# Optimization experiments

Measured on AMD Instinct MI355X. Metric: run time of the kernel, lower is better.

Reference implementation:

```python
import jax, jax.numpy as jnp
import numpy as np
import math

B, T, DIM = 4, 4096, 1024
HID = int(DIM * 1.5)  # 1536
K = 4                  # conv kernel size
S = 16                 # num_slots
D = 384                # slot_dim


def setup_inputs() -> dict:
    key = jax.random.key(0)
    ks = jax.random.split(key, 16)
    inp = {
        "x": jax.random.normal(ks[0], (B, T, DIM), jnp.float32),
        "input_w": jax.random.normal(ks[1], (2 * HID, DIM), jnp.float32) * DIM ** -0.5,
        "conv_w": jax.random.normal(ks[2], (HID, K), jnp.float32) * K ** -0.5,
        "conv_b": jnp.zeros((HID,), jnp.float32),
        "gates_w": jax.random.normal(ks[3], (2 * HID, HID), jnp.float32) * HID ** -0.5,
        "gates_b": jnp.zeros((2 * HID,), jnp.float32),
        "forget_base": jnp.linspace(-4.323, -9.0, HID).astype(jnp.float32),
        "output_w": jax.random.normal(ks[4], (DIM, HID), jnp.float32) * HID ** -0.5,
        "memory_slots": jax.random.normal(ks[5], (S, D), jnp.float32) * 0.02,
        "wq_w": jax.random.normal(ks[6], (D, D), jnp.float32) * 0.02,
        "wk_w": jax.random.normal(ks[7], (D, HID), jnp.float32) * 0.02,
        "wv_w": jax.random.normal(ks[8], (D, HID), jnp.float32) * 0.02,
        "wg_w": jax.random.normal(ks[9], (1, HID), jnp.float32) * 0.02,
        "rq_w": jax.random.normal(ks[10], (D, HID), jnp.float32) * 0.02,
        "rk_w": jax.random.normal(ks[11], (D, D), jnp.float32) * 0.02,
        "rv_w": jax.random.normal(ks[12], (HID, D), jnp.float32) * 0.02,
    }
    return inp


def _causal_dwconv(x, w, b):
    # x: [B,T,H], w: [H,K], b: [H]; torch Conv1d(padding=K-1) then [:, :T] == causal
    xp = jnp.pad(x, ((0, 0), (K - 1, 0), (0, 0)))
    taps = jnp.stack([xp[:, j:j + T, :] for j in range(K)], axis=-1)  # [B,T,H,K]
    return jnp.einsum('bthk,hk->bth', taps, w) + b


def _scan(alpha, x):
    # h_t = alpha_t * h_{t-1} + x_t, elementwise over channels; along axis 1 (time)
    def combine(c1, c2):
        a1, b1 = c1
        a2, b2 = c2
        return a1 * a2, a2 * b1 + b2
    return jax.lax.associative_scan(combine, (alpha, x), axis=1)[1]


def reference(x, input_w, conv_w, conv_b, gates_w, gates_b, forget_base, output_w,
              memory_slots, wq_w, wk_w, wv_w, wg_w, rq_w, rk_w, rv_w):
    L = T // S  # segment length
    proj = x @ input_w.T                       # [B,T,2H]
    gate, xh = proj[..., :HID], proj[..., HID:]
    xh = _causal_dwconv(xh, conv_w, conv_b)    # [B,T,H]
    g = xh @ gates_w.T + gates_b               # [B,T,2H]
    forget, inp = g[..., :HID], g[..., HID:]
    alpha = jnp.exp(-8.0 * jax.nn.softplus(forget_base) * jax.nn.sigmoid(forget))
    xh = jnp.sqrt(1.0 - alpha ** 2 + 1e-6) * jax.nn.sigmoid(inp) * xh
    h = _scan(alpha, xh)                       # [B,T,H]
    xh = gate * jax.nn.sigmoid(gate) * xh      # silu-gated

    # ---- write_memory(xh) ----
    xseg = xh.reshape(B, S, L, HID)
    q = memory_slots @ wq_w.T                  # [S,D]
    kmat = jnp.einsum('bslh,dh->bsld', xseg, wk_w)
    vmat = jnp.einsum('bslh,dh->bsld', xseg, wv_w)
    qk = jnp.einsum('sd,bsld->bsl', q, kmat) / math.sqrt(D)
    attn = jax.nn.softmax(qk, axis=-1)
    mem = jnp.einsum('bsl,bsld->bsd', attn, vmat)  # [B,S,D]

    # ---- read_memory(gelu(xh)*h, mem) ----
    xr = jax.nn.gelu(xh, approximate=False) * h    # [B,T,H]
    rq = xr @ rq_w.T                               # [B,T,D]
    rk = mem @ rk_w.T                              # [B,S,D]
    rv = mem @ rv_w.T                              # [B,S,H]
    qk2 = jnp.einsum('btd,bsd->bts', rq, rk) / math.sqrt(D)
    seg = jnp.arange(T) // L
    mask = seg[:, None] <= jnp.arange(S)[None, :]  # [T,S]
    qk2 = jnp.where(mask[None], qk2, -jnp.inf)
    attn2 = jax.nn.softmax(qk2, axis=-1)
    out = jnp.einsum('bts,bsh->bth', attn2, rv)
    out = jax.nn.sigmoid(xr @ wg_w.T) * out        # write_gate on xr
    return out @ output_w.T                        # [B,T,DIM]
```

## Files before the change

kernel.cpp:

```cpp
#include <hip/hip_runtime.h>
#include <math.h>

#define BB 4
#define TT 4096
#define DIMW 1024
#define HID 1536
#define HID2 3072
#define KC 4
#define SSEG 16
#define LSEG 256
#define DD 384
#define NCH 64
#define CHL 64
#define TH  ((size_t)TT*(size_t)HID)

typedef _Float16 h8 __attribute__((ext_vector_type(8)));
typedef float f4 __attribute__((ext_vector_type(4)));

__device__ __forceinline__ void hsplit(float a, _Float16& h0, _Float16& h1)
{
    _Float16 t = (_Float16)a;
    float tf = (float)t;
    if (fabsf(tf) < 6.103515625e-05f) { t = (_Float16)0.f; tf = 0.f; }
    h0 = t;
    h1 = (_Float16)((a - tf) * 2048.0f);
}

__device__ __forceinline__ void gl_lds16(const _Float16* g, _Float16* l)
{
    __builtin_amdgcn_global_load_lds(
        (const __attribute__((address_space(1))) unsigned int*)g,
        (__attribute__((address_space(3))) unsigned int*)l,
        16, 0, 0);
}

__global__ __launch_bounds__(256) void split2t(const float* __restrict__ src,
                                               _Float16* __restrict__ dst,
                                               int R, int Kd, size_t ps)
{
    __shared__ float tile[64][65];
    const int tid = threadIdx.x;
    const int bx = blockIdx.x;
    const int by = blockIdx.y;
    {
        const int lr = tid >> 2;
        const int lc = (tid & 3) * 16;
        const float* s = src + (size_t)(by * 64 + lr) * Kd + bx * 64 + lc;
#pragma unroll
        for (int e = 0; e < 16; e++) tile[lr][lc + e] = s[e];
    }
    __syncthreads();
    const int c = tid >> 5;
    const int r0 = tid & 31;
#pragma unroll
    for (int rr = 0; rr < 2; rr++) {
        const int r = r0 + rr * 32;
        h8 h0v, h1v;
#pragma unroll
        for (int e = 0; e < 8; e++) {
            _Float16 a0, a1;
            hsplit(tile[r][c * 8 + e], a0, a1);
            h0v[e] = a0; h1v[e] = a1;
        }
        const size_t didx = ((size_t)(bx * 8 + c) * R + by * 64 + r) * 8;
        *(h8*)(dst + didx) = h0v;
        *(h8*)(dst + ps + didx) = h1v;
    }
}

__global__ __launch_bounds__(256) void catkv_kernel(const float* __restrict__ wk,
                                                    const float* __restrict__ wv,
                                                    float* __restrict__ wkv)
{
    const int half = DD * HID;
    int i = blockIdx.x * 256 + threadIdx.x;
    if (i < half) wkv[i] = wk[i];
    else if (i < 2 * half) wkv[i] = wv[i - half];
}

template<int MODE, int TM, int TN>
__global__ __launch_bounds__(256, 2) void gemm_mfma(
    const _Float16* __restrict__ Ap, size_t aps,
    const _Float16* __restrict__ Wp, size_t wps,
    float* __restrict__ C0, float* __restrict__ C1,
    const float* __restrict__ X,
    int M, int Nout, int Kd)
{
    constexpr int MI = TM / 32;
    constexpr int NI = TN / 32;
    constexpr int API = TM / 16;
    constexpr int BPI = TN / 16;
    constexpr int ATOT = 2 * API;
    constexpr int NISS = ATOT + 2 * BPI;

    __shared__ _Float16 Als[2][2][TM * 32];
    __shared__ _Float16 Bls[2][2][TN * 32];

    const int tid = threadIdx.x;
    const int lane = tid & 63;
    const int wv = tid >> 6;
    const int wr = wv >> 1, wc = wv & 1;
    const int lr = lane & 15, lg = lane >> 4;

    int bx = blockIdx.x, by = blockIdx.y;
    {
        const int gx = gridDim.x;
        const int nwg = gx * gridDim.y;
        if ((nwg & 7) == 0) {
            int wg = by * gx + bx;
            wg = (wg & 7) * (nwg >> 3) + (wg >> 3);
            bx = wg % gx; by = wg / gx;
        }
    }
    const int m0 = bx * TM, n0 = by * TN;

    f4 acc1[MI][NI], acc2[MI][NI];
#pragma unroll
    for (int i = 0; i < MI; i++)
#pragma unroll
        for (int j = 0; j < NI; j++) {
            acc1[i][j] = (f4){0.f, 0.f, 0.f, 0.f};
            acc2[i][j] = (f4){0.f, 0.f, 0.f, 0.f};
        }

    auto stage = [&](int kq0, int buf) {
#pragma unroll
        for (int j = 0; j < NISS / 4; j++) {
            const int i = j * 4 + wv;
            if (i < ATOT) {
                const int pl = i / API, s = i - pl * API;
                const int kc = (s * 64) / TM, r0 = (s * 64) % TM;
                const _Float16* g = Ap + pl * aps
                    + ((size_t)(kq0 + kc) * M + m0 + r0) * 8 + lane * 8;
                gl_lds16(g, &Als[buf][pl][(kc * TM + r0) * 8]);
            } else {
                const int jj = i - ATOT;
                const int pl = jj / BPI, s = jj - pl * BPI;
                const int kc = (s * 64) / TN, r0 = (s * 64) % TN;
                const _Float16* g = Wp + pl * wps
                    + ((size_t)(kq0 + kc) * Nout + n0 + r0) * 8 + lane * 8;
                gl_lds16(g, &Bls[buf][pl][(kc * TN + r0) * 8]);
            }
        }
    };

    stage(0, 0);
    __syncthreads();

    const int NS = Kd / 32;
    for (int t = 0; t < NS; t++) {
        const int buf = t & 1;
        if (t + 1 < NS) stage((t + 1) * 4, buf ^ 1);

        h8 af0[MI], af1[MI];
#pragma unroll
        for (int mi = 0; mi < MI; mi++) {
            const int arow = wr * (TM / 2) + mi * 16 + lr;
            af0[mi] = *(const h8*)&Als[buf][0][(lg * TM + arow) * 8];
            af1[mi] = *(const h8*)&Als[buf][1][(lg * TM + arow) * 8];
        }
#pragma unroll
        for (int ni = 0; ni < NI; ni++) {
            const int brow = wc * (TN / 2) + ni * 16 + lr;
            h8 b0 = *(const h8*)&Bls[buf][0][(lg * TN + brow) * 8];
            h8 b1 = *(const h8*)&Bls[buf][1][(lg * TN + brow) * 8];
#pragma unroll
            for (int mi = 0; mi < MI; mi++) {
                acc1[mi][ni] = __builtin_amdgcn_mfma_f32_16x16x32_f16(af0[mi], b0, acc1[mi][ni], 0, 0, 0);
                acc2[mi][ni] = __builtin_amdgcn_mfma_f32_16x16x32_f16(af1[mi], b0, acc2[mi][ni], 0, 0, 0);
                acc2[mi][ni] = __builtin_amdgcn_mfma_f32_16x16x32_f16(af0[mi], b1, acc2[mi][ni], 0, 0, 0);
            }
        }
        __syncthreads();
    }

#pragma unroll
    for (int mi = 0; mi < MI; mi++) {
#pragma unroll
        for (int ni = 0; ni < NI; ni++) {
#pragma unroll
            for (int r = 0; r < 4; r++) {
                const float v = acc1[mi][ni][r] + acc2[mi][ni][r] * 4.8828125e-4f;
                const int m = m0 + wr * (TM / 2) + mi * 16 + lg * 4 + r;
                const int n = n0 + wc * (TN / 2) + ni * 16 + lr;
                if constexpr (MODE == 1) {
                    if (n < HID) C0[(size_t)m * HID + n] = v;
                    else         C1[(size_t)m * HID + (n - HID)] = v;
                } else if constexpr (MODE == 2) {
                    double g = (double)v;
                    double val = (g / (1.0 + exp(-g))) * (double)X[(size_t)m * Nout + n];
                    C0[(size_t)m * Nout + n] = (float)val;
                } else {
                    C0[(size_t)m * Nout + n] = v;
                }
            }
        }
    }
}

template<int MODE, int TM, int TN>
__global__ __launch_bounds__(256) void gemm32(const float* __restrict__ A,
                                              const float* __restrict__ W,
                                              float* __restrict__ C0,
                                              float* __restrict__ C1,
                                              const float* __restrict__ X,
                                              int M, int Nout, int Kd)
{
    constexpr int GM = TM / 64;
    constexpr int GN = TN / 64;
    constexpr int AF4 = TM * 4;
    constexpr int WF4 = TN * 4;
    constexpr int ALOOP = (AF4 + 255) / 256;
    constexpr int WLOOP = (WF4 + 255) / 256;

    __shared__ float As[16][TM];
    __shared__ float Bs[16][TN];

    const int tid = threadIdx.x;
    const int m0 = blockIdx.x * TM;
    const int n0 = blockIdx.y * TN;
    const int tx = tid & 15, ty = tid >> 4;

    float acc[GM * 4][GN * 4];
#pragma unroll
    for (int i = 0; i < GM * 4; i++)
#pragma unroll
        for (int j = 0; j < GN * 4; j++) acc[i][j] = 0.0f;

    float4 aReg[ALOOP], wReg[WLOOP];

    auto issueLoads = [&](int k0) {
#pragma unroll
        for (int u = 0; u < ALOOP; u++) {
            const int idx = tid + u * 256;
            float4 v = make_float4(0.f, 0.f, 0.f, 0.f);
            if (idx < AF4) {
                const int row = idx >> 2, kq = (idx & 3) * 4;
                const long ar = (long)(m0 + row);
                if (ar < M) v = *(const float4*)(A + ar * (long)Kd + (k0 + kq));
            }
            aReg[u] = v;
        }
#pragma unroll
        for (int u = 0; u < WLOOP; u++) {
            const int idx = tid + u * 256;
            float4 v = make_float4(0.f, 0.f, 0.f, 0.f);
            if (idx < WF4) {
                const int row = idx >> 2, kq = (idx & 3) * 4;
                const long wr = (long)(n0 + row);
                v = *(const float4*)(W + wr * (long)Kd + (k0 + kq));
            }
            wReg[u] = v;
        }
    };
    auto writeLDS = [&]() {
#pragma unroll
        for (int u = 0; u < ALOOP; u++) {
            const int idx = tid + u * 256;
            if (idx < AF4) {
                const int row = idx >> 2, kq = (idx & 3) * 4;
                As[kq + 0][row] = aReg[u].x;
                As[kq + 1][row] = aReg[u].y;
                As[kq + 2][row] = aReg[u].z;
                As[kq + 3][row] = aReg[u].w;
            }
        }
#pragma unroll
        for (int u = 0; u < WLOOP; u++) {
            const int idx = tid + u * 256;
            if (idx < WF4) {
                const int row = idx >> 2, kq = (idx & 3) * 4;
                Bs[kq + 0][row] = wReg[u].x;
                Bs[kq + 1][row] = wReg[u].y;
                Bs[kq + 2][row] = wReg[u].z;
                Bs[kq + 3][row] = wReg[u].w;
            }
        }
    };

    issueLoads(0);
    writeLDS();
    __syncthreads();

    const int NT = Kd / 16;
    for (int t = 0; t < NT; t++) {
        if (t + 1 < NT) issueLoads((t + 1) * 16);
#pragma unroll
        for (int k = 0; k < 16; k++) {
            float a[GM * 4], b[GN * 4];
#pragma unroll
            for (int g = 0; g < GM; g++) {
                const float4 t4 = *(const float4*)&As[k][g * 64 + ty * 4];
                a[g * 4 + 0] = t4.x; a[g * 4 + 1] = t4.y;
                a[g * 4 + 2] = t4.z; a[g * 4 + 3] = t4.w;
            }
#pragma unroll
            for (int g = 0; g < GN; g++) {
                const float4 t4 = *(const float4*)&Bs[k][g * 64 + tx * 4];
                b[g * 4 + 0] = t4.x; b[g * 4 + 1] = t4.y;
                b[g * 4 + 2] = t4.z; b[g * 4 + 3] = t4.w;
            }
#pragma unroll
            for (int i = 0; i < GM * 4; i++)
#pragma unroll
                for (int j = 0; j < GN * 4; j++) acc[i][j] += a[i] * b[j];
        }
        __syncthreads();
        if (t + 1 < NT) {
            writeLDS();
            __syncthreads();
        }
    }

#pragma unroll
    for (int i = 0; i < GM * 4; i++) {
        const int m = m0 + (i >> 2) * 64 + ty * 4 + (i & 3);
        if (m >= M) continue;
#pragma unroll
        for (int j = 0; j < GN * 4; j++) {
            const int n = n0 + (j >> 2) * 64 + tx * 4 + (j & 3);
            if (n >= Nout) continue;
            C0[(long)m * Nout + n] = acc[i][j];
        }
    }
}

__global__ __launch_bounds__(256) void spb_kernel(const float* __restrict__ fb,
                                                  double* __restrict__ spb)
{
    int h = blockIdx.x * 256 + threadIdx.x;
    if (h < HID) {
        double xv = (double)fb[h];
        spb[h] = log1p(exp(xv));
    }
}

__global__ __launch_bounds__(256) void conv_kernel(const float* __restrict__ xin,
                                                   const float* __restrict__ cw,
                                                   const float* __restrict__ cb,
                                                   float* __restrict__ outp)
{
    size_t i = (size_t)blockIdx.x * 256 + threadIdx.x;
    if (i >= TH) return;
    int h = (int)(i % HID);
    int t = (int)(i / HID);
    double acc = (double)cb[h];
#pragma unroll
    for (int j = 0; j < KC; j++) {
        int tt = t - (KC - 1) + j;
        if (tt >= 0) acc += (double)cw[h * KC + j] * (double)xin[(size_t)tt * HID + h];
    }
    outp[i] = (float)acc;
}

__global__ __launch_bounds__(256) void alpha_xh2_kernel(float* __restrict__ fg,
                                                        float* __restrict__ ip,
                                                        const float* __restrict__ xh1,
                                                        const double* __restrict__ spb,
                                                        const float* __restrict__ gb)
{
    size_t i = (size_t)blockIdx.x * 256 + threadIdx.x;
    if (i >= TH) return;
    int h = (int)(i % HID);
    double f  = (double)fg[i] + (double)gb[h];
    double g2 = (double)ip[i] + (double)gb[HID + h];
    double sigf = 1.0 / (1.0 + exp(-f));
    double alpha = exp(-8.0 * spb[h] * sigf);
    double s2 = sqrt(1.0 - alpha * alpha + 1e-6);
    double sigi = 1.0 / (1.0 + exp(-g2));
    double x1 = (double)xh1[i];
    fg[i] = (float)alpha;
    ip[i] = (float)(s2 * sigi * x1);
}

__global__ __launch_bounds__(256) void scan1_kernel(const float* __restrict__ alpha,
                                                    const float* __restrict__ xh2,
                                                    double* __restrict__ cA,
                                                    double* __restrict__ cB)
{
    int idx = blockIdx.x * 256 + threadIdx.x;
    if (idx >= NCH * HID) return;
    int h = idx % HID;
    int c = idx / HID;
    size_t base = (size_t)c * CHL * HID + h;
    double aP = 1.0, bV = 0.0;
    for (int i = 0; i < CHL; i++) {
        double a  = (double)alpha[base + (size_t)i * HID];
        double xv = (double)xh2 [base + (size_t)i * HID];
        bV = a * bV + xv;
        aP *= a;
    }
    size_t o = (size_t)c * HID + h;
    cA[o] = aP;
    cB[o] = bV;
}

__global__ __launch_bounds__(256) void scan2_kernel(const double* __restrict__ cA,
                                                    const double* __restrict__ cB,
                                                    double* __restrict__ cH0)
{
    int h = blockIdx.x * 256 + threadIdx.x;
    if (h >= HID) return;
    double carry = 0.0;
    for (int c = 0; c < NCH; c++) {
        size_t o = (size_t)c * HID + h;
        cH0[o] = carry;
        carry = cA[o] * carry + cB[o];
    }
}

__global__ __launch_bounds__(256) void scan3_kernel(const float* __restrict__ alpha,
                                                    const float* __restrict__ xh2,
                                                    const double* __restrict__ cH0,
                                                    float* __restrict__ hout)
{
    int idx = blockIdx.x * 256 + threadIdx.x;
    if (idx >= NCH * HID) return;
    int h = idx % HID;
    int c = idx / HID;
    size_t base = (size_t)c * CHL * HID + h;
    double hv = cH0[(size_t)c * HID + h];
    for (int i = 0; i < CHL; i++) {
        double a  = (double)alpha[base + (size_t)i * HID];
        double xv = (double)xh2 [base + (size_t)i * HID];
        hv = a * hv + xv;
        hout[base + (size_t)i * HID] = (float)hv;
    }
}

__global__ __launch_bounds__(256) void gelu_mul_kernel(float* __restrict__ xh3,
                                                       const float* __restrict__ hbuf)
{
    size_t i = (size_t)blockIdx.x * 256 + threadIdx.x;
    if (i >= TH) return;
    double x3 = (double)xh3[i];
    double ge = 0.5 * x3 * (1.0 + erf(x3 * 0.70710678118654752440));
    xh3[i] = (float)(ge * (double)hbuf[i]);
}

__global__ __launch_bounds__(256) void attn1_kernel(const float* __restrict__ kv,
                                                    const float* __restrict__ qbuf,
                                                    float* __restrict__ mem)
{
    const int s = blockIdx.x;
    const int l = threadIdx.x;
    const size_t row = (size_t)s * LSEG + l;
    const float* kr = kv + row * (2 * DD);
    const float* qs = qbuf + (size_t)s * DD;
    double acc = 0.0;
    for (int d = 0; d < DD; d++) acc += (double)qs[d] * (double)kr[d];
    double qk = acc / sqrt((double)DD);
    __shared__ double r1[256];
    __shared__ double sw[256];
    r1[l] = qk; __syncthreads();
    for (int off = 128; off > 0; off >>= 1) {
        if (l < off) r1[l] = fmax(r1[l], r1[l + off]);
        __syncthreads();
    }
    double m = r1[0]; __syncthreads();
    double e = exp(qk - m);
    r1[l] = e; __syncthreads();
    for (int off = 128; off > 0; off >>= 1) {
        if (l < off) r1[l] += r1[l + off];
        __syncthreads();
    }
    double denom = r1[0];
    sw[l] = e / denom; __syncthreads();
    const size_t vbase = (size_t)s * LSEG * (2 * DD) + DD;
    for (int d = l; d < DD; d += 256) {
        double a2 = 0.0;
        for (int ll = 0; ll < LSEG; ll++)
            a2 += sw[ll] * (double)kv[vbase + (size_t)ll * (2 * DD) + d];
        mem[(size_t)s * DD + d] = (float)a2;
    }
}

__global__ __launch_bounds__(256) void attn2_kernel(const float* __restrict__ rq,
                                                    const float* __restrict__ rk,
                                                    const float* __restrict__ rv,
                                                    const float* __restrict__ xr,
                                                    const float* __restrict__ wg,
                                                    _Float16* __restrict__ outP,
                                                    size_t ps)
{
    const int t = blockIdx.x;
    const int sigma = t >> 8;
    const int tid = threadIdx.x;
    __shared__ double sqk[16];
    __shared__ double red[256];
    __shared__ double sw[16];
    __shared__ double sgate;

    const float* rqn = rq + (size_t)t * DD;
    {
        int s = tid >> 4, j = tid & 15;
        const float* rks = rk + (size_t)s * DD;
        double part = 0.0;
        for (int d = j; d < DD; d += 16) part += (double)rqn[d] * (double)rks[d];
#pragma unroll
        for (int off = 8; off > 0; off >>= 1) part += __shfl_down(part, off, 16);
        if (j == 0) sqk[s] = part;
    }
    double gp = 0.0;
    const float* xrn = xr + (size_t)t * HID;
    for (int hh = tid; hh < HID; hh += 256) gp += (double)xrn[hh] * (double)wg[hh];
    red[tid] = gp; __syncthreads();
    for (int off = 128; off > 0; off >>= 1) {
        if (tid < off) red[tid] += red[tid + off];
        __syncthreads();
    }
    if (tid == 0) {
        const double inv = 1.0 / sqrt((double)DD);
        double m = -1e300;
        for (int ss = sigma; ss < 16; ss++) {
            double v = sqk[ss] * inv;
            sqk[ss] = v;
            if (v > m) m = v;
        }
        double sum = 0.0;
        for (int ss = sigma; ss < 16; ss++) {
            double e = exp(sqk[ss] - m);
            sw[ss] = e;
            sum += e;
        }
        double isum = 1.0 / sum;
        for (int ss = 0; ss < sigma; ss++) sw[ss] = 0.0;
        for (int ss = sigma; ss < 16; ss++) sw[ss] *= isum;
        sgate = 1.0 / (1.0 + exp(-red[0]));
    }
    __syncthreads();
    const double gte = sgate;
    for (int c = tid; c < HID / 8; c += 256) {
        double accv[8] = {0, 0, 0, 0, 0, 0, 0, 0};
        for (int ss = sigma; ss < 16; ss++) {
            const float* rvp = rv + (size_t)ss * HID + c * 8;
            double w = sw[ss];
#pragma unroll
            for (int e = 0; e < 8; e++) accv[e] += w * (double)rvp[e];
        }
        h8 h0v, h1v;
#pragma unroll
        for (int e = 0; e < 8; e++) {
            _Float16 a0, a1;
            hsplit((float)(gte * accv[e]), a0, a1);
            h0v[e] = a0; h1v[e] = a1;
        }
        const size_t didx = ((size_t)c * TT + t) * 8;
        *(h8*)(outP + didx) = h0v;
        *(h8*)(outP + ps + didx) = h1v;
    }
}

extern "C" void kernel_launch(void* const* d_in, const int* in_sizes, int n_in,
                              void* d_out, int out_size, void* d_ws, size_t ws_size,
                              hipStream_t stream)
{
    const float* x            = (const float*)d_in[0];
    const float* input_w      = (const float*)d_in[1];
    const float* conv_w       = (const float*)d_in[2];
    const float* conv_b       = (const float*)d_in[3];
    const float* gates_w      = (const float*)d_in[4];
    const float* gates_b      = (const float*)d_in[5];
    const float* forget_base  = (const float*)d_in[6];
    const float* output_w     = (const float*)d_in[7];
    const float* memory_slots = (const float*)d_in[8];
    const float* wq_w         = (const float*)d_in[9];
    const float* wk_w         = (const float*)d_in[10];
    const float* wv_w         = (const float*)d_in[11];
    const float* wg_w         = (const float*)d_in[12];
    const float* rq_w         = (const float*)d_in[13];
    const float* rk_w         = (const float*)d_in[14];
    const float* rv_w         = (const float*)d_in[15];
    float* out = (float*)d_out;

    double* spb  = (double*)d_ws;
    double* cA   = spb + HID;
    double* cB   = cA + (size_t)NCH * HID;
    double* cH0  = cB + (size_t)NCH * HID;
    float* slotA = (float*)(cH0 + (size_t)NCH * HID);
    float* slotB = slotA + TH;
    float* slotC = slotB + TH;
    float* qbuf   = slotC + TH;
    float* membuf = qbuf + (size_t)SSEG * DD;
    float* rkbuf  = membuf + (size_t)SSEG * DD;
    float* rvbuf  = rkbuf + (size_t)SSEG * DD;

    _Float16* base_h = (_Float16*)(rvbuf + (size_t)SSEG * HID);
    const size_t iwN  = (size_t)HID * DIMW;
    const size_t gwN  = (size_t)HID2 * HID;
    const size_t kvN  = (size_t)(2 * DD) * HID;
    const size_t rqN  = (size_t)DD * HID;
    const size_t owN  = (size_t)DIMW * HID;
    const size_t xbN  = (size_t)TT * DIMW;
    _Float16* iwlo = base_h;
    _Float16* iwhi = iwlo + 2 * iwN;
    _Float16* gwp  = iwhi + 2 * iwN;
    _Float16* wkvp = gwp  + 2 * gwN;
    _Float16* rqwp = wkvp + 2 * kvN;
    _Float16* owp  = rqwp + 2 * rqN;
    _Float16* xbP  = owp  + 2 * owN;
    _Float16* P1   = xbP  + 2 * xbN;

    dim3 blk(256);
    const int ewBlocks = (int)(TH / 256);

    spb_kernel<<<(HID + 255) / 256, blk, 0, stream>>>(forget_base, spb);
    catkv_kernel<<<(2 * DD * HID) / 256, blk, 0, stream>>>(wk_w, wv_w, slotA);
    split2t<<<dim3(DIMW / 64, HID / 64), blk, 0, stream>>>(input_w, iwlo, HID, DIMW, iwN);
    split2t<<<dim3(DIMW / 64, HID / 64), blk, 0, stream>>>(input_w + (size_t)HID * DIMW,
                                                           iwhi, HID, DIMW, iwN);
    split2t<<<dim3(HID / 64, HID2 / 64), blk, 0, stream>>>(gates_w, gwp, HID2, HID, gwN);
    split2t<<<dim3(HID / 64, (2 * DD) / 64), blk, 0, stream>>>(slotA, wkvp, 2 * DD, HID, kvN);
    split2t<<<dim3(HID / 64, DD / 64), blk, 0, stream>>>(rq_w, rqwp, DD, HID, rqN);
    split2t<<<dim3(HID / 64, DIMW / 64), blk, 0, stream>>>(output_w, owp, DIMW, HID, owN);
    gemm32<0, 64, 64><<<dim3(1, DD / 64), blk, 0, stream>>>(
        memory_slots, wq_w, qbuf, (float*)nullptr, (const float*)nullptr, SSEG, DD, DD);

    for (int b = 0; b < BB; b++) {
        const float* xb   = x   + (size_t)b * TT * DIMW;
        float*       outb = out + (size_t)b * TT * DIMW;

        split2t<<<dim3(DIMW / 64, TT / 64), blk, 0, stream>>>(xb, xbP, TT, DIMW, xbN);
        gemm_mfma<0, 128, 128><<<dim3(TT / 128, HID / 128), blk, 0, stream>>>(
            xbP, xbN, iwhi, iwN, slotB, (float*)nullptr, (const float*)nullptr,
            TT, HID, DIMW);
        conv_kernel<<<ewBlocks, blk, 0, stream>>>(slotB, conv_w, conv_b, slotC);
        split2t<<<dim3(HID / 64, TT / 64), blk, 0, stream>>>(slotC, P1, TT, HID, TH);
        gemm_mfma<1, 128, 128><<<dim3(TT / 128, HID2 / 128), blk, 0, stream>>>(
            P1, TH, gwp, gwN, slotA, slotB, (const float*)nullptr, TT, HID2, HID);
        alpha_xh2_kernel<<<ewBlocks, blk, 0, stream>>>(slotA, slotB, slotC, spb, gates_b);
        scan1_kernel<<<(NCH * HID) / 256, blk, 0, stream>>>(slotA, slotB, cA, cB);
        scan2_kernel<<<(HID + 255) / 256, blk, 0, stream>>>(cA, cB, cH0);
        scan3_kernel<<<(NCH * HID) / 256, blk, 0, stream>>>(slotA, slotB, cH0, slotC);
        gemm_mfma<2, 128, 128><<<dim3(TT / 128, HID / 128), blk, 0, stream>>>(
            xbP, xbN, iwlo, iwN, slotA, (float*)nullptr, slotB, TT, HID, DIMW);
        split2t<<<dim3(HID / 64, TT / 64), blk, 0, stream>>>(slotA, P1, TT, HID, TH);
        gemm_mfma<0, 128, 64><<<dim3(TT / 128, (2 * DD) / 64), blk, 0, stream>>>(
            P1, TH, wkvp, kvN, slotB, (float*)nullptr, (const float*)nullptr,
            TT, 2 * DD, HID);
        attn1_kernel<<<SSEG, blk, 0, stream>>>(slotB, qbuf, membuf);
        gelu_mul_kernel<<<ewBlocks, blk, 0, stream>>>(slotA, slotC);
        split2t<<<dim3(HID / 64, TT / 64), blk, 0, stream>>>(slotA, P1, TT, HID, TH);
        gemm_mfma<0, 64, 64><<<dim3(TT / 64, DD / 64), blk, 0, stream>>>(
            P1, TH, rqwp, rqN, slotB, (float*)nullptr, (const float*)nullptr,
            TT, DD, HID);
        gemm32<0, 64, 64><<<dim3(1, DD / 64), blk, 0, stream>>>(
            membuf, rk_w, rkbuf, (float*)nullptr, (const float*)nullptr, SSEG, DD, DD);
        gemm32<0, 64, 64><<<dim3(1, HID / 64), blk, 0, stream>>>(
            membuf, rv_w, rvbuf, (float*)nullptr, (const float*)nullptr, SSEG, HID, DD);
        attn2_kernel<<<TT, blk, 0, stream>>>(slotB, rkbuf, rvbuf, slotA, wg_w, P1, TH);
        gemm_mfma<0, 128, 128><<<dim3(TT / 128, DIMW / 128), blk, 0, stream>>>(
            P1, TH, owp, owN, outb, (float*)nullptr, (const float*)nullptr,
            TT, DIMW, HID);
    }
}
```

Baseline: 2.660 ms.

## Fuse fp16 split into producer kernels and enlarge MFMA GEMM tiles

The fp32-to-split-fp16 transposed packing is folded into the conv, gelu_mul and MODE-2 GEMM epilogues, which removes three separate split2t passes and their extra full-size reads. The GEMM template gains configurable wave grids, so 512-thread 256x128 and 256x256 tiles can be used for the large projections. Tiles too big for two accumulator sets fold the low-part correction into a single accumulator each step. This saves memory traffic and raises per-block reuse, but the fused epilogues write scattered 2-byte stores, the large tiles increase register pressure, and the per-step correction fold changes rounding slightly.

New measurement: 2.736 ms. +2.8%, slower.

```diff
diff --git a/kernel.cpp b/kernel.cpp
--- a/kernel.cpp
+++ b/kernel.cpp
@@ -17,6 +17,8 @@
 typedef _Float16 h8 __attribute__((ext_vector_type(8)));
 typedef float f4 __attribute__((ext_vector_type(4)));
 
+#define RSCL 4.8828125e-4f
+
 __device__ __forceinline__ void hsplit(float a, _Float16& h0, _Float16& h1)
 {
     _Float16 t = (_Float16)a;
@@ -78,20 +80,24 @@
     else if (i < 2 * half) wkv[i] = wv[i - half];
 }
 
-template<int MODE, int TM, int TN>
-__global__ __launch_bounds__(256, 2) void gemm_mfma(
+template<int MODE, int TM, int TN, int WRN, int WCN>
+__global__ __launch_bounds__(WRN * WCN * 64, 2) void gemm_mfma(
     const _Float16* __restrict__ Ap, size_t aps,
     const _Float16* __restrict__ Wp, size_t wps,
     float* __restrict__ C0, float* __restrict__ C1,
     const float* __restrict__ X,
+    _Float16* __restrict__ OP, size_t ops,
     int M, int Nout, int Kd)
 {
-    constexpr int MI = TM / 32;
-    constexpr int NI = TN / 32;
+    constexpr int NWAVE = WRN * WCN;
+    constexpr int WTM = TM / WRN, WTN = TN / WCN;
+    constexpr int MI = WTM / 16, NI = WTN / 16;
     constexpr int API = TM / 16;
     constexpr int BPI = TN / 16;
     constexpr int ATOT = 2 * API;
     constexpr int NISS = ATOT + 2 * BPI;
+    static_assert(NISS % NWAVE == 0, "issue count must divide waves");
+    constexpr bool DUAL = (MI * NI <= 16);
 
     __shared__ _Float16 Als[2][2][TM * 32];
     __shared__ _Float16 Bls[2][2][TN * 32];
@@ -99,7 +105,7 @@
     const int tid = threadIdx.x;
     const int lane = tid & 63;
     const int wv = tid >> 6;
-    const int wr = wv >> 1, wc = wv & 1;
+    const int wr = wv / WCN, wc = wv % WCN;
     const int lr = lane & 15, lg = lane >> 4;
 
     int bx = blockIdx.x, by = blockIdx.y;
@@ -120,13 +126,13 @@
 #pragma unroll
         for (int j = 0; j < NI; j++) {
             acc1[i][j] = (f4){0.f, 0.f, 0.f, 0.f};
-            acc2[i][j] = (f4){0.f, 0.f, 0.f, 0.f};
+            if constexpr (DUAL) acc2[i][j] = (f4){0.f, 0.f, 0.f, 0.f};
         }
 
     auto stage = [&](int kq0, int buf) {
 #pragma unroll
-        for (int j = 0; j < NISS / 4; j++) {
-            const int i = j * 4 + wv;
+        for (int j = 0; j < NISS / NWAVE; j++) {
+            const int i = j * NWAVE + wv;
             if (i < ATOT) {
                 const int pl = i / API, s = i - pl * API;
                 const int kc = (s * 64) / TM, r0 = (s * 64) % TM;
@@ -155,20 +161,27 @@
         h8 af0[MI], af1[MI];
 #pragma unroll
         for (int mi = 0; mi < MI; mi++) {
-            const int arow = wr * (TM / 2) + mi * 16 + lr;
+            const int arow = wr * WTM + mi * 16 + lr;
             af0[mi] = *(const h8*)&Als[buf][0][(lg * TM + arow) * 8];
             af1[mi] = *(const h8*)&Als[buf][1][(lg * TM + arow) * 8];
         }
 #pragma unroll
         for (int ni = 0; ni < NI; ni++) {
-            const int brow = wc * (TN / 2) + ni * 16 + lr;
+            const int brow = wc * WTN + ni * 16 + lr;
             h8 b0 = *(const h8*)&Bls[buf][0][(lg * TN + brow) * 8];
             h8 b1 = *(const h8*)&Bls[buf][1][(lg * TN + brow) * 8];
 #pragma unroll
             for (int mi = 0; mi < MI; mi++) {
                 acc1[mi][ni] = __builtin_amdgcn_mfma_f32_16x16x32_f16(af0[mi], b0, acc1[mi][ni], 0, 0, 0);
-                acc2[mi][ni] = __builtin_amdgcn_mfma_f32_16x16x32_f16(af1[mi], b0, acc2[mi][ni], 0, 0, 0);
-                acc2[mi][ni] = __builtin_amdgcn_mfma_f32_16x16x32_f16(af0[mi], b1, acc2[mi][ni], 0, 0, 0);
+                if constexpr (DUAL) {
+                    acc2[mi][ni] = __builtin_amdgcn_mfma_f32_16x16x32_f16(af1[mi], b0, acc2[mi][ni], 0, 0, 0);
+                    acc2[mi][ni] = __builtin_amdgcn_mfma_f32_16x16x32_f16(af0[mi], b1, acc2[mi][ni], 0, 0, 0);
+                } else {
+                    f4 tmp = (f4){0.f, 0.f, 0.f, 0.f};
+                    tmp = __builtin_amdgcn_mfma_f32_16x16x32_f16(af1[mi], b0, tmp, 0, 0, 0);
+                    tmp = __builtin_amdgcn_mfma_f32_16x16x32_f16(af0[mi], b1, tmp, 0, 0, 0);
+                    acc1[mi][ni] = acc1[mi][ni] + tmp * RSCL;
+                }
             }
         }
         __syncthreads();
@@ -180,16 +193,23 @@
         for (int ni = 0; ni < NI; ni++) {
 #pragma unroll
             for (int r = 0; r < 4; r++) {
-                const float v = acc1[mi][ni][r] + acc2[mi][ni][r] * 4.8828125e-4f;
-                const int m = m0 + wr * (TM / 2) + mi * 16 + lg * 4 + r;
-                const int n = n0 + wc * (TN / 2) + ni * 16 + lr;
+                float v;
+                if constexpr (DUAL) v = acc1[mi][ni][r] + acc2[mi][ni][r] * RSCL;
+                else                v = acc1[mi][ni][r];
+                const int m = m0 + wr * WTM + mi * 16 + lg * 4 + r;
+                const int n = n0 + wc * WTN + ni * 16 + lr;
                 if constexpr (MODE == 1) {
                     if (n < HID) C0[(size_t)m * HID + n] = v;
                     else         C1[(size_t)m * HID + (n - HID)] = v;
                 } else if constexpr (MODE == 2) {
                     double g = (double)v;
-                    double val = (g / (1.0 + exp(-g))) * (double)X[(size_t)m * Nout + n];
-                    C0[(size_t)m * Nout + n] = (float)val;
+                    float fv = (float)((g / (1.0 + exp(-g))) * (double)X[(size_t)m * Nout + n]);
+                    C0[(size_t)m * Nout + n] = fv;
+                    _Float16 a0, a1;
+                    hsplit(fv, a0, a1);
+                    const size_t didx = ((size_t)(n >> 3) * M + m) * 8 + (n & 7);
+                    OP[didx] = a0;
+                    OP[ops + didx] = a1;
                 } else {
                     C0[(size_t)m * Nout + n] = v;
                 }
@@ -338,7 +358,9 @@
 __global__ __launch_bounds__(256) void conv_kernel(const float* __restrict__ xin,
                                                    const float* __restrict__ cw,
                                                    const float* __restrict__ cb,
-                                                   float* __restrict__ outp)
+                                                   float* __restrict__ outp,
+                                                   _Float16* __restrict__ outP,
+                                                   size_t ps)
 {
     size_t i = (size_t)blockIdx.x * 256 + threadIdx.x;
     if (i >= TH) return;
@@ -350,7 +372,13 @@
         int tt = t - (KC - 1) + j;
         if (tt >= 0) acc += (double)cw[h * KC + j] * (double)xin[(size_t)tt * HID + h];
     }
-    outp[i] = (float)acc;
+    float fv = (float)acc;
+    outp[i] = fv;
+    _Float16 a0, a1;
+    hsplit(fv, a0, a1);
+    const size_t didx = ((size_t)(h >> 3) * TT + t) * 8 + (h & 7);
+    outP[didx] = a0;
+    outP[ps + didx] = a1;
 }
 
 __global__ __launch_bounds__(256) void alpha_xh2_kernel(float* __restrict__ fg,
@@ -429,13 +457,23 @@
 }
 
 __global__ __launch_bounds__(256) void gelu_mul_kernel(float* __restrict__ xh3,
-                                                       const float* __restrict__ hbuf)
+                                                       const float* __restrict__ hbuf,
+                                                       _Float16* __restrict__ outP,
+                                                       size_t ps)
 {
     size_t i = (size_t)blockIdx.x * 256 + threadIdx.x;
     if (i >= TH) return;
+    int h = (int)(i % HID);
+    int t = (int)(i / HID);
     double x3 = (double)xh3[i];
     double ge = 0.5 * x3 * (1.0 + erf(x3 * 0.70710678118654752440));
-    xh3[i] = (float)(ge * (double)hbuf[i]);
+    float fv = (float)(ge * (double)hbuf[i]);
+    xh3[i] = fv;
+    _Float16 a0, a1;
+    hsplit(fv, a0, a1);
+    const size_t didx = ((size_t)(h >> 3) * TT + t) * 8 + (h & 7);
+    outP[didx] = a0;
+    outP[ps + didx] = a1;
 }
 
 __global__ __launch_bounds__(256) void attn1_kernel(const float* __restrict__ kv,
@@ -602,6 +640,7 @@
     _Float16* P1   = xbP  + 2 * xbN;
 
     dim3 blk(256);
+    dim3 blk512(512);
     const int ewBlocks = (int)(TH / 256);
 
     spb_kernel<<<(HID + 255) / 256, blk, 0, stream>>>(forget_base, spb);
@@ -621,36 +660,34 @@
         float*       outb = out + (size_t)b * TT * DIMW;
 
         split2t<<<dim3(DIMW / 64, TT / 64), blk, 0, stream>>>(xb, xbP, TT, DIMW, xbN);
-        gemm_mfma<0, 128, 128><<<dim3(TT / 128, HID / 128), blk, 0, stream>>>(
+        gemm_mfma<0, 256, 128, 4, 2><<<dim3(TT / 256, HID / 128), blk512, 0, stream>>>(
             xbP, xbN, iwhi, iwN, slotB, (float*)nullptr, (const float*)nullptr,
-            TT, HID, DIMW);
-        conv_kernel<<<ewBlocks, blk, 0, stream>>>(slotB, conv_w, conv_b, slotC);
-        split2t<<<dim3(HID / 64, TT / 64), blk, 0, stream>>>(slotC, P1, TT, HID, TH);
-        gemm_mfma<1, 128, 128><<<dim3(TT / 128, HID2 / 128), blk, 0, stream>>>(
-            P1, TH, gwp, gwN, slotA, slotB, (const float*)nullptr, TT, HID2, HID);
+            (_Float16*)nullptr, 0, TT, HID, DIMW);
+        conv_kernel<<<ewBlocks, blk, 0, stream>>>(slotB, conv_w, conv_b, slotC, P1, TH);
+        gemm_mfma<1, 256, 256, 4, 2><<<dim3(TT / 256, HID2 / 256), blk512, 0, stream>>>(
+            P1, TH, gwp, gwN, slotA, slotB, (const float*)nullptr,
+            (_Float16*)nullptr, 0, TT, HID2, HID);
         alpha_xh2_kernel<<<ewBlocks, blk, 0, stream>>>(slotA, slotB, slotC, spb, gates_b);
         scan1_kernel<<<(NCH * HID) / 256, blk, 0, stream>>>(slotA, slotB, cA, cB);
         scan2_kernel<<<(HID + 255) / 256, blk, 0, stream>>>(cA, cB, cH0);
         scan3_kernel<<<(NCH * HID) / 256, blk, 0, stream>>>(slotA, slotB, cH0, slotC);
-        gemm_mfma<2, 128, 128><<<dim3(TT / 128, HID / 128), blk, 0, stream>>>(
-            xbP, xbN, iwlo, iwN, slotA, (float*)nullptr, slotB, TT, HID, DIMW);
-        split2t<<<dim3(HID / 64, TT / 64), blk, 0, stream>>>(slotA, P1, TT, HID, TH);
-        gemm_mfma<0, 128, 64><<<dim3(TT / 128, (2 * DD) / 64), blk, 0, stream>>>(
+        gemm_mfma<2, 256, 128, 4, 2><<<dim3(TT / 256, HID / 128), blk512, 0, stream>>>(
+            xbP, xbN, iwlo, iwN, slotA, (float*)nullptr, slotB, P1, TH, TT, HID, DIMW);
+        gemm_mfma<0, 128, 128, 2, 2><<<dim3(TT / 128, (2 * DD) / 128), blk, 0, stream>>>(
             P1, TH, wkvp, kvN, slotB, (float*)nullptr, (const float*)nullptr,
-            TT, 2 * DD, HID);
+            (_Float16*)nullptr, 0, TT, 2 * DD, HID);
         attn1_kernel<<<SSEG, blk, 0, stream>>>(slotB, qbuf, membuf);
-        gelu_mul_kernel<<<ewBlocks, blk, 0, stream>>>(slotA, slotC);
-        split2t<<<dim3(HID / 64, TT / 64), blk, 0, stream>>>(slotA, P1, TT, HID, TH);
-        gemm_mfma<0, 64, 64><<<dim3(TT / 64, DD / 64), blk, 0, stream>>>(
+        gelu_mul_kernel<<<ewBlocks, blk, 0, stream>>>(slotA, slotC, P1, TH);
+        gemm_mfma<0, 128, 128, 2, 2><<<dim3(TT / 128, DD / 128), blk, 0, stream>>>(
             P1, TH, rqwp, rqN, slotB, (float*)nullptr, (const float*)nullptr,
-            TT, DD, HID);
+            (_Float16*)nullptr, 0, TT, DD, HID);
         gemm32<0, 64, 64><<<dim3(1, DD / 64), blk, 0, stream>>>(
             membuf, rk_w, rkbuf, (float*)nullptr, (const float*)nullptr, SSEG, DD, DD);
         gemm32<0, 64, 64><<<dim3(1, HID / 64), blk, 0, stream>>>(
             membuf, rv_w, rvbuf, (float*)nullptr, (const float*)nullptr, SSEG, HID, DD);
         attn2_kernel<<<TT, blk, 0, stream>>>(slotB, rkbuf, rvbuf, slotA, wg_w, P1, TH);
-        gemm_mfma<0, 128, 128><<<dim3(TT / 128, DIMW / 128), blk, 0, stream>>>(
+        gemm_mfma<0, 128, 128, 2, 2><<<dim3(TT / 128, DIMW / 128), blk, 0, stream>>>(
             P1, TH, owp, owN, outb, (float*)nullptr, (const float*)nullptr,
-            TT, DIMW, HID);
-    }
-}
+            (_Float16*)nullptr, 0, TT, DIMW, HID);
+    }
+}
```
